# Performance work log

Hardware: AMD Instinct MI355X
Metric: run time of the kernel (lower is better)

## Reference

```python
import jax, jax.numpy as jnp
import numpy as np

N, K = 200000, 16
C_IN = 4           # in_channels (head stage)
H1, H2 = 16, 32    # nbr_hidden_channels//2, nbr_hidden_channels
C_OUT = 64         # channel_list[0]
HEAD = 256         # head_channels
EPS = 1e-5


def _bn(x, g, b):
    # train-mode BatchNorm1d over the row (point/neighbor) axis
    m = jnp.mean(x, axis=0)
    v = jnp.var(x, axis=0)
    return (x - m) * jax.lax.rsqrt(v + EPS) * g + b


def setup_inputs() -> dict:
    key = jax.random.key(0)
    ks = jax.random.split(key, 8)

    def lin(k, fan_in, fan_out):
        bound = 1.0 / np.sqrt(fan_in)  # torch Linear default init
        return jax.random.uniform(k, (fan_in, fan_out), minval=-bound, maxval=bound, dtype=jnp.float32)

    return {
        "p": jax.random.normal(ks[0], (N, 3), dtype=jnp.float32),
        "f": jax.random.normal(ks[1], (N, C_IN), dtype=jnp.float32),
        "group_idx": jax.random.randint(ks[2], (N, K), 0, N),
        "w1": lin(ks[3], 3 + C_IN, H1),
        "g1": jnp.ones((H1,), jnp.float32),
        "b1": jnp.zeros((H1,), jnp.float32),
        "w2": lin(ks[4], H1, H2),
        "g2": jnp.ones((H2,), jnp.float32),
        "b2": jnp.zeros((H2,), jnp.float32),
        "w3": lin(ks[5], H2, C_OUT),
        "g_nbr": 0.8 * jnp.ones((C_OUT,), jnp.float32),  # nn.init.constant_(nbr_bn.weight, 0.8)
        "b_nbr": jnp.zeros((C_OUT,), jnp.float32),
        "g_post": jnp.ones((C_OUT,), jnp.float32),       # (channel_list[0]/out_channels)**0.5 == 1.0
        "b_post": jnp.zeros((C_OUT,), jnp.float32),
        "w_post": lin(ks[6], C_OUT, HEAD),
    }


def reference(p, f, group_idx, w1, g1, b1, w2, g2, b2, w3, g_nbr, b_nbr, g_post, b_post, w_post):
    # neighbor gather: relative coords and features  -> (N, K, 3), (N, K, C_IN)
    p_nbr = p[group_idx] - p[:, None, :]
    f_nbr = f[group_idx]
    x = jnp.concatenate([p_nbr, f_nbr], axis=-1).reshape(N * K, 3 + C_IN)
    # nbr_embed: Linear-BN-GELU x2 + Linear (all no-bias linears)
    x = jax.nn.gelu(_bn(x @ w1, g1, b1), approximate=False)
    x = jax.nn.gelu(_bn(x @ w2, g2, b2), approximate=False)
    x = (x @ w3).reshape(N, K, C_OUT).max(axis=1)  # max-pool over K neighbors
    # nbr_proj is Identity for the head stage; nbr_bn then f = f_nbr
    x = _bn(x, g_nbr, b_nbr)
    # post_proj: BN + Linear(C_OUT -> HEAD, no bias)
    out = _bn(x, g_post, b_post) @ w_post
    return out
```

## Files before the change

kernel.cpp:

```cpp
#include <hip/hip_runtime.h>
#include <cmath>

#define NPTS  200000
#define KNBR  16
#define MROWS 3200000
#define EPSB  1e-5f
#define H2LD  260

__device__ __forceinline__ float gelu_f(float x) {
    return 0.5f * x * (1.0f + erff(x * 0.70710678118654752f));
}

__global__ __launch_bounds__(256) void k_pack(
    const float* __restrict__ p, const float4* __restrict__ f,
    float4* __restrict__ pk)
{
    int n = blockIdx.x * 256 + threadIdx.x;
    if (n < NPTS) {
        float4 a;
        a.x = p[n * 3 + 0]; a.y = p[n * 3 + 1]; a.z = p[n * 3 + 2]; a.w = 0.f;
        pk[2 * n]     = a;
        pk[2 * n + 1] = f[n];
    }
}

__global__ __launch_bounds__(256) void k_stats1(
    const float4* __restrict__ pk, const int* __restrict__ gidx,
    float* __restrict__ stats)
{
    __shared__ float red[4 * 35];

    float acc[35];
#pragma unroll
    for (int c = 0; c < 35; c++) acc[c] = 0.f;

    int stride = gridDim.x * 256;
    for (int r = blockIdx.x * 256 + threadIdx.x; r < MROWS; r += stride) {
        int n = r >> 4;
        int idx = gidx[r];
        float4 pa = pk[2 * idx];
        float4 fb = pk[2 * idx + 1];
        float4 pc = pk[2 * n];
        float x[7];
        x[0] = pa.x - pc.x; x[1] = pa.y - pc.y; x[2] = pa.z - pc.z;
        x[3] = fb.x; x[4] = fb.y; x[5] = fb.z; x[6] = fb.w;
#pragma unroll
        for (int i = 0; i < 7; i++) acc[i] += x[i];
        int t = 7;
#pragma unroll
        for (int i = 0; i < 7; i++)
#pragma unroll
            for (int l = i; l < 7; l++) { acc[t] = fmaf(x[i], x[l], acc[t]); t++; }
    }
    int lane = threadIdx.x & 63, wv = threadIdx.x >> 6;
#pragma unroll
    for (int c = 0; c < 35; c++) {
        float v = acc[c];
        v += __shfl_down(v, 32); v += __shfl_down(v, 16); v += __shfl_down(v, 8);
        v += __shfl_down(v, 4);  v += __shfl_down(v, 2);  v += __shfl_down(v, 1);
        if (lane == 0) red[wv * 35 + c] = v;
    }
    __syncthreads();
    for (int c = threadIdx.x; c < 35; c += 256)
        atomicAdd(&stats[c], red[c] + red[35 + c] + red[70 + c] + red[105 + c]);
}

__global__ void k_fin1(const float* __restrict__ stats, const float* __restrict__ w1,
                       const float* __restrict__ g, const float* __restrict__ b,
                       float* __restrict__ scsh)
{
    int j = threadIdx.x;
    if (j < 16) {
        const float invM = 1.0f / (float)MROWS;
        float w[7];
#pragma unroll
        for (int i = 0; i < 7; i++) w[i] = w1[i * 16 + j];
        float m = 0.f;
#pragma unroll
        for (int i = 0; i < 7; i++) m = fmaf(w[i], stats[i], m);
        m *= invM;
        float e2 = 0.f;
        int t = 7;
#pragma unroll
        for (int i = 0; i < 7; i++)
#pragma unroll
            for (int l = i; l < 7; l++) {
                float coeff = (i == l) ? 1.0f : 2.0f;
                e2 = fmaf(coeff * w[i] * w[l], stats[t], e2);
                t++;
            }
        e2 *= invM;
        float v = e2 - m * m;
        float sc = g[j] * rsqrtf(v + EPSB);
        scsh[j] = sc;
        scsh[16 + j] = fmaf(-m, sc, b[j]);
    }
}

__global__ __launch_bounds__(256) void k_stats2a(
    const float4* __restrict__ pk, const int* __restrict__ gidx,
    const float* __restrict__ w1, const float* __restrict__ scsh1,
    float* __restrict__ stats)
{
    __shared__ __align__(16) float w1s[112];
    __shared__ float sc1s[16], sh1s[16];
    __shared__ float red[4 * 81];
    for (int i = threadIdx.x; i < 112; i += 256) w1s[i] = w1[i];
    if (threadIdx.x < 16) {
        sc1s[threadIdx.x] = scsh1[threadIdx.x];
        sh1s[threadIdx.x] = scsh1[16 + threadIdx.x];
    }
    __syncthreads();
    const float4* w1v = (const float4*)w1s;

    float acc[81];
#pragma unroll
    for (int c = 0; c < 81; c++) acc[c] = 0.f;

    int stride = gridDim.x * 256;
    for (int r = blockIdx.x * 256 + threadIdx.x; r < MROWS; r += stride) {
        int n = r >> 4;
        int idx = gidx[r];
        float4 pa = pk[2 * idx];
        float4 fb = pk[2 * idx + 1];
        float4 pc = pk[2 * n];
        float x[7];
        x[0] = pa.x - pc.x; x[1] = pa.y - pc.y; x[2] = pa.z - pc.z;
        x[3] = fb.x; x[4] = fb.y; x[5] = fb.z; x[6] = fb.w;
        float h1[16];
#pragma unroll
        for (int j0 = 0; j0 < 16; j0 += 4) {
            float y0 = 0.f, y1 = 0.f, y2 = 0.f, y3 = 0.f;
#pragma unroll
            for (int i = 0; i < 7; i++) {
                float4 w = w1v[i * 4 + (j0 >> 2)];
                float xi = x[i];
                y0 = fmaf(xi, w.x, y0); y1 = fmaf(xi, w.y, y1);
                y2 = fmaf(xi, w.z, y2); y3 = fmaf(xi, w.w, y3);
            }
            h1[j0 + 0] = gelu_f(fmaf(y0, sc1s[j0 + 0], sh1s[j0 + 0]));
            h1[j0 + 1] = gelu_f(fmaf(y1, sc1s[j0 + 1], sh1s[j0 + 1]));
            h1[j0 + 2] = gelu_f(fmaf(y2, sc1s[j0 + 2], sh1s[j0 + 2]));
            h1[j0 + 3] = gelu_f(fmaf(y3, sc1s[j0 + 3], sh1s[j0 + 3]));
        }
        int t = 0;
#pragma unroll
        for (int i = 0; i < 6; i++)
#pragma unroll
            for (int l = i; l < 16; l++) { acc[t] = fmaf(h1[i], h1[l], acc[t]); t++; }
    }
    int lane = threadIdx.x & 63, wv = threadIdx.x >> 6;
#pragma unroll
    for (int c = 0; c < 81; c++) {
        float v = acc[c];
        v += __shfl_down(v, 32); v += __shfl_down(v, 16); v += __shfl_down(v, 8);
        v += __shfl_down(v, 4);  v += __shfl_down(v, 2);  v += __shfl_down(v, 1);
        if (lane == 0) red[wv * 81 + c] = v;
    }
    __syncthreads();
    for (int c = threadIdx.x; c < 81; c += 256)
        atomicAdd(&stats[c], red[c] + red[81 + c] + red[162 + c] + red[243 + c]);
}

__global__ __launch_bounds__(256) void k_stats2b(
    const float4* __restrict__ pk, const int* __restrict__ gidx,
    const float* __restrict__ w1, const float* __restrict__ scsh1,
    float* __restrict__ stats)
{
    __shared__ __align__(16) float w1s[112];
    __shared__ float sc1s[16], sh1s[16];
    __shared__ float red[4 * 71];
    for (int i = threadIdx.x; i < 112; i += 256) w1s[i] = w1[i];
    if (threadIdx.x < 16) {
        sc1s[threadIdx.x] = scsh1[threadIdx.x];
        sh1s[threadIdx.x] = scsh1[16 + threadIdx.x];
    }
    __syncthreads();
    const float4* w1v = (const float4*)w1s;

    float acc[71];
#pragma unroll
    for (int c = 0; c < 71; c++) acc[c] = 0.f;

    int stride = gridDim.x * 256;
    for (int r = blockIdx.x * 256 + threadIdx.x; r < MROWS; r += stride) {
        int n = r >> 4;
        int idx = gidx[r];
        float4 pa = pk[2 * idx];
        float4 fb = pk[2 * idx + 1];
        float4 pc = pk[2 * n];
        float x[7];
        x[0] = pa.x - pc.x; x[1] = pa.y - pc.y; x[2] = pa.z - pc.z;
        x[3] = fb.x; x[4] = fb.y; x[5] = fb.z; x[6] = fb.w;
        float h1[16];
#pragma unroll
        for (int j0 = 0; j0 < 16; j0 += 4) {
            float y0 = 0.f, y1 = 0.f, y2 = 0.f, y3 = 0.f;
#pragma unroll
            for (int i = 0; i < 7; i++) {
                float4 w = w1v[i * 4 + (j0 >> 2)];
                float xi = x[i];
                y0 = fmaf(xi, w.x, y0); y1 = fmaf(xi, w.y, y1);
                y2 = fmaf(xi, w.z, y2); y3 = fmaf(xi, w.w, y3);
            }
            h1[j0 + 0] = gelu_f(fmaf(y0, sc1s[j0 + 0], sh1s[j0 + 0]));
            h1[j0 + 1] = gelu_f(fmaf(y1, sc1s[j0 + 1], sh1s[j0 + 1]));
            h1[j0 + 2] = gelu_f(fmaf(y2, sc1s[j0 + 2], sh1s[j0 + 2]));
            h1[j0 + 3] = gelu_f(fmaf(y3, sc1s[j0 + 3], sh1s[j0 + 3]));
        }
#pragma unroll
        for (int i = 0; i < 16; i++) acc[i] += h1[i];
        int t = 16;
#pragma unroll
        for (int i = 6; i < 16; i++)
#pragma unroll
            for (int l = i; l < 16; l++) { acc[t] = fmaf(h1[i], h1[l], acc[t]); t++; }
    }
    int lane = threadIdx.x & 63, wv = threadIdx.x >> 6;
#pragma unroll
    for (int c = 0; c < 71; c++) {
        float v = acc[c];
        v += __shfl_down(v, 32); v += __shfl_down(v, 16); v += __shfl_down(v, 8);
        v += __shfl_down(v, 4);  v += __shfl_down(v, 2);  v += __shfl_down(v, 1);
        if (lane == 0) red[wv * 71 + c] = v;
    }
    __syncthreads();
    for (int c = threadIdx.x; c < 71; c += 256)
        atomicAdd(&stats[81 + c], red[c] + red[71 + c] + red[142 + c] + red[213 + c]);
}

__global__ void k_fin2(const float* __restrict__ stats, const float* __restrict__ w2,
                       const float* __restrict__ g, const float* __restrict__ b,
                       float* __restrict__ scsh)
{
    int j = threadIdx.x;
    if (j < 32) {
        const float invM = 1.0f / (float)MROWS;
        float w[16];
#pragma unroll
        for (int i = 0; i < 16; i++) w[i] = w2[i * 32 + j];
        float m = 0.f;
#pragma unroll
        for (int i = 0; i < 16; i++) m = fmaf(w[i], stats[81 + i], m);
        m *= invM;
        float e2 = 0.f;
        int t = 0;
#pragma unroll
        for (int i = 0; i < 6; i++)
#pragma unroll
            for (int l = i; l < 16; l++) {
                float coeff = (i == l) ? 1.0f : 2.0f;
                e2 = fmaf(coeff * w[i] * w[l], stats[t], e2);
                t++;
            }
        t = 97;
#pragma unroll
        for (int i = 6; i < 16; i++)
#pragma unroll
            for (int l = i; l < 16; l++) {
                float coeff = (i == l) ? 1.0f : 2.0f;
                e2 = fmaf(coeff * w[i] * w[l], stats[t], e2);
                t++;
            }
        e2 *= invM;
        float v = e2 - m * m;
        float sc = g[j] * rsqrtf(v + EPSB);
        scsh[j] = sc;
        scsh[32 + j] = fmaf(-m, sc, b[j]);
    }
}

__global__ __launch_bounds__(256) void k_pool2(
    const float* __restrict__ p, const float4* __restrict__ f,
    const int* __restrict__ gidx,
    const float* __restrict__ w1, const float* __restrict__ w2,
    const float* __restrict__ w3,
    const float* __restrict__ scsh1, const float* __restrict__ scsh2,
    float* __restrict__ stats, float* __restrict__ pooled)
{
    __shared__ __align__(16) float w1s[112];
    __shared__ __align__(16) float w2s[512];
    __shared__ __align__(16) float w3s[2048];
    __shared__ __align__(16) float h2t[32 * H2LD];
    __shared__ float sc1s[16], sh1s[16], sc2s[32], sh2s[32];
    __shared__ float reds[256];
    __shared__ float redq[256];
    int tid = threadIdx.x;
    for (int i = tid; i < 112; i += 256) w1s[i] = w1[i];
    for (int i = tid; i < 512; i += 256) w2s[i] = w2[i];
    for (int i = tid; i < 2048; i += 256) w3s[i] = w3[i];
    if (tid < 16) { sc1s[tid] = scsh1[tid]; sh1s[tid] = scsh1[16 + tid]; }
    if (tid < 32) { sc2s[tid] = scsh2[tid]; sh2s[tid] = scsh2[32 + tid]; }
    __syncthreads();

    const float4* w1v = (const float4*)w1s;
    const float4* w2v = (const float4*)w2s;
    const float4* w3v = (const float4*)w3s;

    int lane = tid & 63;
    int pt = tid >> 4;
    int cc = tid & 15;

    float s0 = 0.f, s1 = 0.f, s2 = 0.f, s3 = 0.f;
    float q0 = 0.f, q1 = 0.f, q2 = 0.f, q3 = 0.f;

#pragma unroll 1
    for (int it = 0; it < 4; it++) {
        int r = it * 800000 + blockIdx.x * 256 + tid;
        int n = r >> 4;
        int idx = gidx[r];
        float4 fv = f[idx];
        float x[7];
        x[0] = p[idx * 3 + 0] - p[n * 3 + 0];
        x[1] = p[idx * 3 + 1] - p[n * 3 + 1];
        x[2] = p[idx * 3 + 2] - p[n * 3 + 2];
        x[3] = fv.x; x[4] = fv.y; x[5] = fv.z; x[6] = fv.w;

        float h1[16];
#pragma unroll
        for (int j0 = 0; j0 < 16; j0 += 4) {
            float y0 = 0.f, y1 = 0.f, y2 = 0.f, y3 = 0.f;
#pragma unroll
            for (int i = 0; i < 7; i++) {
                float4 w = w1v[i * 4 + (j0 >> 2)];
                float xi = x[i];
                y0 = fmaf(xi, w.x, y0); y1 = fmaf(xi, w.y, y1);
                y2 = fmaf(xi, w.z, y2); y3 = fmaf(xi, w.w, y3);
            }
            h1[j0 + 0] = gelu_f(fmaf(y0, sc1s[j0 + 0], sh1s[j0 + 0]));
            h1[j0 + 1] = gelu_f(fmaf(y1, sc1s[j0 + 1], sh1s[j0 + 1]));
            h1[j0 + 2] = gelu_f(fmaf(y2, sc1s[j0 + 2], sh1s[j0 + 2]));
            h1[j0 + 3] = gelu_f(fmaf(y3, sc1s[j0 + 3], sh1s[j0 + 3]));
        }
#pragma unroll
        for (int j0 = 0; j0 < 32; j0 += 4) {
            float y0 = 0.f, y1 = 0.f, y2 = 0.f, y3 = 0.f;
#pragma unroll
            for (int i = 0; i < 16; i++) {
                float4 w = w2v[i * 8 + (j0 >> 2)];
                float hi = h1[i];
                y0 = fmaf(hi, w.x, y0); y1 = fmaf(hi, w.y, y1);
                y2 = fmaf(hi, w.z, y2); y3 = fmaf(hi, w.w, y3);
            }
            h2t[(j0 + 0) * H2LD + tid] = gelu_f(fmaf(y0, sc2s[j0 + 0], sh2s[j0 + 0]));
            h2t[(j0 + 1) * H2LD + tid] = gelu_f(fmaf(y1, sc2s[j0 + 1], sh2s[j0 + 1]));
            h2t[(j0 + 2) * H2LD + tid] = gelu_f(fmaf(y2, sc2s[j0 + 2], sh2s[j0 + 2]));
            h2t[(j0 + 3) * H2LD + tid] = gelu_f(fmaf(y3, sc2s[j0 + 3], sh2s[j0 + 3]));
        }
        __syncthreads();

        float m0 = -3.0e38f, m1 = -3.0e38f, m2 = -3.0e38f, m3 = -3.0e38f;
#pragma unroll 1
        for (int qd = 0; qd < 4; qd++) {
            int rb = (pt << 4) + (qd << 2);
            float a00 = 0.f, a01 = 0.f, a02 = 0.f, a03 = 0.f;
            float a10 = 0.f, a11 = 0.f, a12 = 0.f, a13 = 0.f;
            float a20 = 0.f, a21 = 0.f, a22 = 0.f, a23 = 0.f;
            float a30 = 0.f, a31 = 0.f, a32 = 0.f, a33 = 0.f;
#pragma unroll 8
            for (int i = 0; i < 32; i++) {
                float4 hv = *(const float4*)&h2t[i * H2LD + rb];
                float4 wf = w3v[i * 16 + cc];
                a00 = fmaf(hv.x, wf.x, a00); a01 = fmaf(hv.x, wf.y, a01);
                a02 = fmaf(hv.x, wf.z, a02); a03 = fmaf(hv.x, wf.w, a03);
                a10 = fmaf(hv.y, wf.x, a10); a11 = fmaf(hv.y, wf.y, a11);
                a12 = fmaf(hv.y, wf.z, a12); a13 = fmaf(hv.y, wf.w, a13);
                a20 = fmaf(hv.z, wf.x, a20); a21 = fmaf(hv.z, wf.y, a21);
                a22 = fmaf(hv.z, wf.z, a22); a23 = fmaf(hv.z, wf.w, a23);
                a30 = fmaf(hv.w, wf.x, a30); a31 = fmaf(hv.w, wf.y, a31);
                a32 = fmaf(hv.w, wf.z, a32); a33 = fmaf(hv.w, wf.w, a33);
            }
            m0 = fmaxf(fmaxf(fmaxf(m0, a00), fmaxf(a10, a20)), a30);
            m1 = fmaxf(fmaxf(fmaxf(m1, a01), fmaxf(a11, a21)), a31);
            m2 = fmaxf(fmaxf(fmaxf(m2, a02), fmaxf(a12, a22)), a32);
            m3 = fmaxf(fmaxf(fmaxf(m3, a03), fmaxf(a13, a23)), a33);
        }
        int np = it * 50000 + blockIdx.x * 16 + pt;
        *(float4*)&pooled[(size_t)np * 64 + cc * 4] = make_float4(m0, m1, m2, m3);
        s0 += m0; q0 = fmaf(m0, m0, q0);
        s1 += m1; q1 = fmaf(m1, m1, q1);
        s2 += m2; q2 = fmaf(m2, m2, q2);
        s3 += m3; q3 = fmaf(m3, m3, q3);
        __syncthreads();
    }

    s0 += __shfl_down(s0, 32); s0 += __shfl_down(s0, 16);
    s1 += __shfl_down(s1, 32); s1 += __shfl_down(s1, 16);
    s2 += __shfl_down(s2, 32); s2 += __shfl_down(s2, 16);
    s3 += __shfl_down(s3, 32); s3 += __shfl_down(s3, 16);
    q0 += __shfl_down(q0, 32); q0 += __shfl_down(q0, 16);
    q1 += __shfl_down(q1, 32); q1 += __shfl_down(q1, 16);
    q2 += __shfl_down(q2, 32); q2 += __shfl_down(q2, 16);
    q3 += __shfl_down(q3, 32); q3 += __shfl_down(q3, 16);
    int wv = tid >> 6;
    if (lane < 16) {
        reds[wv * 64 + lane * 4 + 0] = s0;
        reds[wv * 64 + lane * 4 + 1] = s1;
        reds[wv * 64 + lane * 4 + 2] = s2;
        reds[wv * 64 + lane * 4 + 3] = s3;
        redq[wv * 64 + lane * 4 + 0] = q0;
        redq[wv * 64 + lane * 4 + 1] = q1;
        redq[wv * 64 + lane * 4 + 2] = q2;
        redq[wv * 64 + lane * 4 + 3] = q3;
    }
    __syncthreads();
    if (tid < 64) {
        atomicAdd(&stats[tid],
                  reds[tid] + reds[64 + tid] + reds[128 + tid] + reds[192 + tid]);
        atomicAdd(&stats[64 + tid],
                  redq[tid] + redq[64 + tid] + redq[128 + tid] + redq[192 + tid]);
    }
}

__global__ void k_fin3(const float* __restrict__ stats,
                       const float* __restrict__ g_nbr, const float* __restrict__ g_post,
                       const float* __restrict__ b_post, float* __restrict__ scsh)
{
    int j = threadIdx.x;
    if (j < 64) {
        float m = stats[j] * (1.0f / NPTS);
        float v = stats[64 + j] * (1.0f / NPTS) - m * m;
        float a1 = g_nbr[j] * rsqrtf(v + EPSB);
        float s3 = g_post[j] * a1 * rsqrtf(fmaf(a1 * a1, v, EPSB));
        scsh[j] = s3;
        scsh[64 + j] = fmaf(-m, s3, b_post[j]);
    }
}

__global__ __launch_bounds__(256) void k_head(
    const float* __restrict__ pooled, const float* __restrict__ scsh3,
    const float* __restrict__ wpost, float* __restrict__ out)
{
    __shared__ float rowbuf[512];
    __shared__ float s3s[64], c3s[64];
    int tid = threadIdx.x;
    if (tid < 64) { s3s[tid] = scsh3[tid]; c3s[tid] = scsh3[64 + tid]; }
    float wcol[64];
#pragma unroll
    for (int j = 0; j < 64; j++) wcol[j] = wpost[j * 256 + tid];
    __syncthreads();

    const int nchunks = NPTS / 8;
    for (int c = blockIdx.x; c < nchunks; c += gridDim.x) {
        int n0 = c * 8;
#pragma unroll
        for (int t = tid; t < 512; t += 256) {
            int rr = t >> 6, j = t & 63;
            rowbuf[t] = fmaf(pooled[(size_t)(n0 + rr) * 64 + j], s3s[j], c3s[j]);
        }
        __syncthreads();
#pragma unroll
        for (int rr = 0; rr < 8; rr++) {
            float acc = 0.f;
#pragma unroll
            for (int j = 0; j < 64; j++) acc = fmaf(rowbuf[rr * 64 + j], wcol[j], acc);
            out[(size_t)(n0 + rr) * 256 + tid] = acc;
        }
        __syncthreads();
    }
}

extern "C" void kernel_launch(void* const* d_in, const int* in_sizes, int n_in,
                              void* d_out, int out_size, void* d_ws, size_t ws_size,
                              hipStream_t stream)
{
    const float*  p    = (const float*)d_in[0];
    const float4* f    = (const float4*)d_in[1];
    const int*    gidx = (const int*)d_in[2];
    const float*  w1   = (const float*)d_in[3];
    const float*  g1   = (const float*)d_in[4];
    const float*  b1   = (const float*)d_in[5];
    const float*  w2   = (const float*)d_in[6];
    const float*  g2   = (const float*)d_in[7];
    const float*  b2   = (const float*)d_in[8];
    const float*  w3   = (const float*)d_in[9];
    const float*  gn   = (const float*)d_in[10];
    const float*  gp   = (const float*)d_in[12];
    const float*  bp   = (const float*)d_in[13];
    const float*  wp   = (const float*)d_in[14];
    float* out = (float*)d_out;
    float* ws  = (float*)d_ws;

    float* stats1 = ws;
    float* scsh1  = ws + 40;
    float* stats2 = ws + 80;
    float* scsh2  = ws + 240;
    float* stats3 = ws + 304;
    float* scsh3  = ws + 432;
    float* pooled = ws + 1024;
    float4* pk    = (float4*)(ws + 1024);

    hipMemsetAsync(d_ws, 0, 2048, stream);
    k_pack<<<(NPTS + 255) / 256, 256, 0, stream>>>(p, f, pk);
    k_stats1<<<2048, 256, 0, stream>>>(pk, gidx, stats1);
    k_fin1<<<1, 64, 0, stream>>>(stats1, w1, g1, b1, scsh1);
    k_stats2a<<<2048, 256, 0, stream>>>(pk, gidx, w1, scsh1, stats2);
    k_stats2b<<<2048, 256, 0, stream>>>(pk, gidx, w1, scsh1, stats2);
    k_fin2<<<1, 64, 0, stream>>>(stats2, w2, g2, b2, scsh2);
    k_pool2<<<3125, 256, 0, stream>>>(p, f, gidx, w1, w2, w3, scsh1, scsh2, stats3, pooled);
    k_fin3<<<1, 64, 0, stream>>>(stats3, gn, gp, bp, scsh3);
    k_head<<<1024, 256, 0, stream>>>(pooled, scsh3, wp, out);
}
```

Measured before the change: 1.287 ms.

## Materialize first-layer pre-activations once and reuse across stats and pool passes

The first linear layer's 16-channel output per neighbor row is computed once and stored in workspace in a transposed, coalesced layout. The layer-1 BN statistics now come directly from per-channel sums instead of the 7x7 input moment trick. The later moment passes and the pooling kernel read this buffer instead of repeating the random neighbor gather and layer-1 matmul. In exchange the code writes and then reads about 205 MB of extra traffic three times, and falls back to the old gather path when the workspace is too small.

```diff
diff --git a/kernel.cpp b/kernel.cpp
--- a/kernel.cpp
+++ b/kernel.cpp
@@ -24,18 +24,25 @@
     }
 }
 
-__global__ __launch_bounds__(256) void k_stats1(
+__global__ __launch_bounds__(256) void k_gy1(
     const float4* __restrict__ pk, const int* __restrict__ gidx,
-    float* __restrict__ stats)
-{
-    __shared__ float red[4 * 35];
-
-    float acc[35];
-#pragma unroll
-    for (int c = 0; c < 35; c++) acc[c] = 0.f;
-
+    const float* __restrict__ w1, float* __restrict__ stats,
+    float* __restrict__ y1d)
+{
+    __shared__ __align__(16) float w1s[112];
+    __shared__ float red[4 * 32];
+    for (int i = threadIdx.x; i < 112; i += 256) w1s[i] = w1[i];
+    __syncthreads();
+    const float4* w1v = (const float4*)w1s;
+
+    float acc[32];
+#pragma unroll
+    for (int c = 0; c < 32; c++) acc[c] = 0.f;
+
+    int tid = threadIdx.x;
+    int lr = tid & 63;
     int stride = gridDim.x * 256;
-    for (int r = blockIdx.x * 256 + threadIdx.x; r < MROWS; r += stride) {
+    for (int r = blockIdx.x * 256 + tid; r < MROWS; r += stride) {
         int n = r >> 4;
         int idx = gidx[r];
         float4 pa = pk[2 * idx];
@@ -44,90 +51,7 @@
         float x[7];
         x[0] = pa.x - pc.x; x[1] = pa.y - pc.y; x[2] = pa.z - pc.z;
         x[3] = fb.x; x[4] = fb.y; x[5] = fb.z; x[6] = fb.w;
-#pragma unroll
-        for (int i = 0; i < 7; i++) acc[i] += x[i];
-        int t = 7;
-#pragma unroll
-        for (int i = 0; i < 7; i++)
-#pragma unroll
-            for (int l = i; l < 7; l++) { acc[t] = fmaf(x[i], x[l], acc[t]); t++; }
-    }
-    int lane = threadIdx.x & 63, wv = threadIdx.x >> 6;
-#pragma unroll
-    for (int c = 0; c < 35; c++) {
-        float v = acc[c];
-        v += __shfl_down(v, 32); v += __shfl_down(v, 16); v += __shfl_down(v, 8);
-        v += __shfl_down(v, 4);  v += __shfl_down(v, 2);  v += __shfl_down(v, 1);
-        if (lane == 0) red[wv * 35 + c] = v;
-    }
-    __syncthreads();
-    for (int c = threadIdx.x; c < 35; c += 256)
-        atomicAdd(&stats[c], red[c] + red[35 + c] + red[70 + c] + red[105 + c]);
-}
-
-__global__ void k_fin1(const float* __restrict__ stats, const float* __restrict__ w1,
-                       const float* __restrict__ g, const float* __restrict__ b,
-                       float* __restrict__ scsh)
-{
-    int j = threadIdx.x;
-    if (j < 16) {
-        const float invM = 1.0f / (float)MROWS;
-        float w[7];
-#pragma unroll
-        for (int i = 0; i < 7; i++) w[i] = w1[i * 16 + j];
-        float m = 0.f;
-#pragma unroll
-        for (int i = 0; i < 7; i++) m = fmaf(w[i], stats[i], m);
-        m *= invM;
-        float e2 = 0.f;
-        int t = 7;
-#pragma unroll
-        for (int i = 0; i < 7; i++)
-#pragma unroll
-            for (int l = i; l < 7; l++) {
-                float coeff = (i == l) ? 1.0f : 2.0f;
-                e2 = fmaf(coeff * w[i] * w[l], stats[t], e2);
-                t++;
-            }
-        e2 *= invM;
-        float v = e2 - m * m;
-        float sc = g[j] * rsqrtf(v + EPSB);
-        scsh[j] = sc;
-        scsh[16 + j] = fmaf(-m, sc, b[j]);
-    }
-}
-
-__global__ __launch_bounds__(256) void k_stats2a(
-    const float4* __restrict__ pk, const int* __restrict__ gidx,
-    const float* __restrict__ w1, const float* __restrict__ scsh1,
-    float* __restrict__ stats)
-{
-    __shared__ __align__(16) float w1s[112];
-    __shared__ float sc1s[16], sh1s[16];
-    __shared__ float red[4 * 81];
-    for (int i = threadIdx.x; i < 112; i += 256) w1s[i] = w1[i];
-    if (threadIdx.x < 16) {
-        sc1s[threadIdx.x] = scsh1[threadIdx.x];
-        sh1s[threadIdx.x] = scsh1[16 + threadIdx.x];
-    }
-    __syncthreads();
-    const float4* w1v = (const float4*)w1s;
-
-    float acc[81];
-#pragma unroll
-    for (int c = 0; c < 81; c++) acc[c] = 0.f;
-
-    int stride = gridDim.x * 256;
-    for (int r = blockIdx.x * 256 + threadIdx.x; r < MROWS; r += stride) {
-        int n = r >> 4;
-        int idx = gidx[r];
-        float4 pa = pk[2 * idx];
-        float4 fb = pk[2 * idx + 1];
-        float4 pc = pk[2 * n];
-        float x[7];
-        x[0] = pa.x - pc.x; x[1] = pa.y - pc.y; x[2] = pa.z - pc.z;
-        x[3] = fb.x; x[4] = fb.y; x[5] = fb.z; x[6] = fb.w;
-        float h1[16];
+        float* yb = y1d + (size_t)(r >> 6) * 1024 + lr;
 #pragma unroll
         for (int j0 = 0; j0 < 16; j0 += 4) {
             float y0 = 0.f, y1 = 0.f, y2 = 0.f, y3 = 0.f;
@@ -138,18 +62,73 @@
                 y0 = fmaf(xi, w.x, y0); y1 = fmaf(xi, w.y, y1);
                 y2 = fmaf(xi, w.z, y2); y3 = fmaf(xi, w.w, y3);
             }
-            h1[j0 + 0] = gelu_f(fmaf(y0, sc1s[j0 + 0], sh1s[j0 + 0]));
-            h1[j0 + 1] = gelu_f(fmaf(y1, sc1s[j0 + 1], sh1s[j0 + 1]));
-            h1[j0 + 2] = gelu_f(fmaf(y2, sc1s[j0 + 2], sh1s[j0 + 2]));
-            h1[j0 + 3] = gelu_f(fmaf(y3, sc1s[j0 + 3], sh1s[j0 + 3]));
-        }
+            yb[(j0 + 0) * 64] = y0; yb[(j0 + 1) * 64] = y1;
+            yb[(j0 + 2) * 64] = y2; yb[(j0 + 3) * 64] = y3;
+            acc[j0 + 0] += y0; acc[16 + j0 + 0] += y0 * y0;
+            acc[j0 + 1] += y1; acc[16 + j0 + 1] += y1 * y1;
+            acc[j0 + 2] += y2; acc[16 + j0 + 2] += y2 * y2;
+            acc[j0 + 3] += y3; acc[16 + j0 + 3] += y3 * y3;
+        }
+    }
+    int lane = tid & 63, wv = tid >> 6;
+#pragma unroll
+    for (int c = 0; c < 32; c++) {
+        float v = acc[c];
+        v += __shfl_down(v, 32); v += __shfl_down(v, 16); v += __shfl_down(v, 8);
+        v += __shfl_down(v, 4);  v += __shfl_down(v, 2);  v += __shfl_down(v, 1);
+        if (lane == 0) red[wv * 32 + c] = v;
+    }
+    __syncthreads();
+    for (int c = tid; c < 32; c += 256)
+        atomicAdd(&stats[c], red[c] + red[32 + c] + red[64 + c] + red[96 + c]);
+}
+
+__global__ void k_fin1b(const float* __restrict__ stats, const float* __restrict__ g,
+                        const float* __restrict__ b, float* __restrict__ scsh)
+{
+    int j = threadIdx.x;
+    if (j < 16) {
+        const float invM = 1.0f / (float)MROWS;
+        float m = stats[j] * invM;
+        float v = stats[16 + j] * invM - m * m;
+        float sc = g[j] * rsqrtf(v + EPSB);
+        scsh[j] = sc;
+        scsh[16 + j] = fmaf(-m, sc, b[j]);
+    }
+}
+
+__global__ __launch_bounds__(256) void k_momA(
+    const float* __restrict__ y1d, const float* __restrict__ scsh1,
+    float* __restrict__ stats)
+{
+    __shared__ float sc1s[16], sh1s[16];
+    __shared__ float red[4 * 81];
+    if (threadIdx.x < 16) {
+        sc1s[threadIdx.x] = scsh1[threadIdx.x];
+        sh1s[threadIdx.x] = scsh1[16 + threadIdx.x];
+    }
+    __syncthreads();
+
+    float acc[81];
+#pragma unroll
+    for (int c = 0; c < 81; c++) acc[c] = 0.f;
+
+    int tid = threadIdx.x;
+    int lr = tid & 63;
+    int stride = gridDim.x * 256;
+    for (int r = blockIdx.x * 256 + tid; r < MROWS; r += stride) {
+        const float* yb = y1d + (size_t)(r >> 6) * 1024 + lr;
+        float h1[16];
+#pragma unroll
+        for (int j = 0; j < 16; j++)
+            h1[j] = gelu_f(fmaf(yb[j * 64], sc1s[j], sh1s[j]));
         int t = 0;
 #pragma unroll
         for (int i = 0; i < 6; i++)
 #pragma unroll
             for (int l = i; l < 16; l++) { acc[t] = fmaf(h1[i], h1[l], acc[t]); t++; }
     }
-    int lane = threadIdx.x & 63, wv = threadIdx.x >> 6;
+    int lane = tid & 63, wv = tid >> 6;
 #pragma unroll
     for (int c = 0; c < 81; c++) {
         float v = acc[c];
@@ -158,56 +137,35 @@
         if (lane == 0) red[wv * 81 + c] = v;
     }
     __syncthreads();
-    for (int c = threadIdx.x; c < 81; c += 256)
+    for (int c = tid; c < 81; c += 256)
         atomicAdd(&stats[c], red[c] + red[81 + c] + red[162 + c] + red[243 + c]);
 }
 
-__global__ __launch_bounds__(256) void k_stats2b(
-    const float4* __restrict__ pk, const int* __restrict__ gidx,
-    const float* __restrict__ w1, const float* __restrict__ scsh1,
+__global__ __launch_bounds__(256) void k_momB(
+    const float* __restrict__ y1d, const float* __restrict__ scsh1,
     float* __restrict__ stats)
 {
-    __shared__ __align__(16) float w1s[112];
     __shared__ float sc1s[16], sh1s[16];
     __shared__ float red[4 * 71];
-    for (int i = threadIdx.x; i < 112; i += 256) w1s[i] = w1[i];
     if (threadIdx.x < 16) {
         sc1s[threadIdx.x] = scsh1[threadIdx.x];
         sh1s[threadIdx.x] = scsh1[16 + threadIdx.x];
     }
     __syncthreads();
-    const float4* w1v = (const float4*)w1s;
 
     float acc[71];
 #pragma unroll
     for (int c = 0; c < 71; c++) acc[c] = 0.f;
 
+    int tid = threadIdx.x;
+    int lr = tid & 63;
     int stride = gridDim.x * 256;
-    for (int r = blockIdx.x * 256 + threadIdx.x; r < MROWS; r += stride) {
-        int n = r >> 4;
-        int idx = gidx[r];
-        float4 pa = pk[2 * idx];
-        float4 fb = pk[2 * idx + 1];
-        float4 pc = pk[2 * n];
-        float x[7];
-        x[0] = pa.x - pc.x; x[1] = pa.y - pc.y; x[2] = pa.z - pc.z;
-        x[3] = fb.x; x[4] = fb.y; x[5] = fb.z; x[6] = fb.w;
+    for (int r = blockIdx.x * 256 + tid; r < MROWS; r += stride) {
+        const float* yb = y1d + (size_t)(r >> 6) * 1024 + lr;
         float h1[16];
 #pragma unroll
-        for (int j0 = 0; j0 < 16; j0 += 4) {
-            float y0 = 0.f, y1 = 0.f, y2 = 0.f, y3 = 0.f;
-#pragma unroll
-            for (int i = 0; i < 7; i++) {
-                float4 w = w1v[i * 4 + (j0 >> 2)];
-                float xi = x[i];
-                y0 = fmaf(xi, w.x, y0); y1 = fmaf(xi, w.y, y1);
-                y2 = fmaf(xi, w.z, y2); y3 = fmaf(xi, w.w, y3);
-            }
-            h1[j0 + 0] = gelu_f(fmaf(y0, sc1s[j0 + 0], sh1s[j0 + 0]));
-            h1[j0 + 1] = gelu_f(fmaf(y1, sc1s[j0 + 1], sh1s[j0 + 1]));
-            h1[j0 + 2] = gelu_f(fmaf(y2, sc1s[j0 + 2], sh1s[j0 + 2]));
-            h1[j0 + 3] = gelu_f(fmaf(y3, sc1s[j0 + 3], sh1s[j0 + 3]));
-        }
+        for (int j = 0; j < 16; j++)
+            h1[j] = gelu_f(fmaf(yb[j * 64], sc1s[j], sh1s[j]));
 #pragma unroll
         for (int i = 0; i < 16; i++) acc[i] += h1[i];
         int t = 16;
@@ -216,7 +174,7 @@
 #pragma unroll
             for (int l = i; l < 16; l++) { acc[t] = fmaf(h1[i], h1[l], acc[t]); t++; }
     }
-    int lane = threadIdx.x & 63, wv = threadIdx.x >> 6;
+    int lane = tid & 63, wv = tid >> 6;
 #pragma unroll
     for (int c = 0; c < 71; c++) {
         float v = acc[c];
@@ -225,7 +183,7 @@
         if (lane == 0) red[wv * 71 + c] = v;
     }
     __syncthreads();
-    for (int c = threadIdx.x; c < 71; c += 256)
+    for (int c = tid; c < 71; c += 256)
         atomicAdd(&stats[81 + c], red[c] + red[71 + c] + red[142 + c] + red[213 + c]);
 }
 
@@ -270,15 +228,12 @@
     }
 }
 
-__global__ __launch_bounds__(256) void k_pool2(
-    const float* __restrict__ p, const float4* __restrict__ f,
-    const int* __restrict__ gidx,
-    const float* __restrict__ w1, const float* __restrict__ w2,
-    const float* __restrict__ w3,
+__global__ __launch_bounds__(256) void k_pool2y(
+    const float* __restrict__ y1d,
+    const float* __restrict__ w2, const float* __restrict__ w3,
     const float* __restrict__ scsh1, const float* __restrict__ scsh2,
     float* __restrict__ stats, float* __restrict__ pooled)
 {
-    __shared__ __align__(16) float w1s[112];
     __shared__ __align__(16) float w2s[512];
     __shared__ __align__(16) float w3s[2048];
     __shared__ __align__(16) float h2t[32 * H2LD];
@@ -286,14 +241,12 @@
     __shared__ float reds[256];
     __shared__ float redq[256];
     int tid = threadIdx.x;
-    for (int i = tid; i < 112; i += 256) w1s[i] = w1[i];
     for (int i = tid; i < 512; i += 256) w2s[i] = w2[i];
     for (int i = tid; i < 2048; i += 256) w3s[i] = w3[i];
     if (tid < 16) { sc1s[tid] = scsh1[tid]; sh1s[tid] = scsh1[16 + tid]; }
     if (tid < 32) { sc2s[tid] = scsh2[tid]; sh2s[tid] = scsh2[32 + tid]; }
     __syncthreads();
 
-    const float4* w1v = (const float4*)w1s;
     const float4* w2v = (const float4*)w2s;
     const float4* w3v = (const float4*)w3s;
 
@@ -307,31 +260,11 @@
 #pragma unroll 1
     for (int it = 0; it < 4; it++) {
         int r = it * 800000 + blockIdx.x * 256 + tid;
-        int n = r >> 4;
-        int idx = gidx[r];
-        float4 fv = f[idx];
-        float x[7];
-        x[0] = p[idx * 3 + 0] - p[n * 3 + 0];
-        x[1] = p[idx * 3 + 1] - p[n * 3 + 1];
-        x[2] = p[idx * 3 + 2] - p[n * 3 + 2];
-        x[3] = fv.x; x[4] = fv.y; x[5] = fv.z; x[6] = fv.w;
-
+        const float* yb = y1d + (size_t)(r >> 6) * 1024 + lane;
         float h1[16];
 #pragma unroll
-        for (int j0 = 0; j0 < 16; j0 += 4) {
-            float y0 = 0.f, y1 = 0.f, y2 = 0.f, y3 = 0.f;
-#pragma unroll
-            for (int i = 0; i < 7; i++) {
-                float4 w = w1v[i * 4 + (j0 >> 2)];
-                float xi = x[i];
-                y0 = fmaf(xi, w.x, y0); y1 = fmaf(xi, w.y, y1);
-                y2 = fmaf(xi, w.z, y2); y3 = fmaf(xi, w.w, y3);
-            }
-            h1[j0 + 0] = gelu_f(fmaf(y0, sc1s[j0 + 0], sh1s[j0 + 0]));
-            h1[j0 + 1] = gelu_f(fmaf(y1, sc1s[j0 + 1], sh1s[j0 + 1]));
-            h1[j0 + 2] = gelu_f(fmaf(y2, sc1s[j0 + 2], sh1s[j0 + 2]));
-            h1[j0 + 3] = gelu_f(fmaf(y3, sc1s[j0 + 3], sh1s[j0 + 3]));
-        }
+        for (int j = 0; j < 16; j++)
+            h1[j] = gelu_f(fmaf(yb[j * 64], sc1s[j], sh1s[j]));
 #pragma unroll
         for (int j0 = 0; j0 < 32; j0 += 4) {
             float y0 = 0.f, y1 = 0.f, y2 = 0.f, y3 = 0.f;
@@ -412,6 +345,297 @@
     }
 }
 
+__global__ __launch_bounds__(256) void k_s1g(
+    const float4* __restrict__ pk, const int* __restrict__ gidx,
+    float* __restrict__ stats)
+{
+    __shared__ float red[4 * 35];
+    float acc[35];
+#pragma unroll
+    for (int c = 0; c < 35; c++) acc[c] = 0.f;
+    int stride = gridDim.x * 256;
+    for (int r = blockIdx.x * 256 + threadIdx.x; r < MROWS; r += stride) {
+        int n = r >> 4;
+        int idx = gidx[r];
+        float4 pa = pk[2 * idx];
+        float4 fb = pk[2 * idx + 1];
+        float4 pc = pk[2 * n];
+        float x[7];
+        x[0] = pa.x - pc.x; x[1] = pa.y - pc.y; x[2] = pa.z - pc.z;
+        x[3] = fb.x; x[4] = fb.y; x[5] = fb.z; x[6] = fb.w;
+#pragma unroll
+        for (int i = 0; i < 7; i++) acc[i] += x[i];
+        int t = 7;
+#pragma unroll
+        for (int i = 0; i < 7; i++)
+#pragma unroll
+            for (int l = i; l < 7; l++) { acc[t] = fmaf(x[i], x[l], acc[t]); t++; }
+    }
+    int lane = threadIdx.x & 63, wv = threadIdx.x >> 6;
+#pragma unroll
+    for (int c = 0; c < 35; c++) {
+        float v = acc[c];
+        v += __shfl_down(v, 32); v += __shfl_down(v, 16); v += __shfl_down(v, 8);
+        v += __shfl_down(v, 4);  v += __shfl_down(v, 2);  v += __shfl_down(v, 1);
+        if (lane == 0) red[wv * 35 + c] = v;
+    }
+    __syncthreads();
+    for (int c = threadIdx.x; c < 35; c += 256)
+        atomicAdd(&stats[c], red[c] + red[35 + c] + red[70 + c] + red[105 + c]);
+}
+
+__global__ void k_f1g(const float* __restrict__ stats, const float* __restrict__ w1,
+                      const float* __restrict__ g, const float* __restrict__ b,
+                      float* __restrict__ scsh)
+{
+    int j = threadIdx.x;
+    if (j < 16) {
+        const float invM = 1.0f / (float)MROWS;
+        float w[7];
+#pragma unroll
+        for (int i = 0; i < 7; i++) w[i] = w1[i * 16 + j];
+        float m = 0.f;
+#pragma unroll
+        for (int i = 0; i < 7; i++) m = fmaf(w[i], stats[i], m);
+        m *= invM;
+        float e2 = 0.f;
+        int t = 7;
+#pragma unroll
+        for (int i = 0; i < 7; i++)
+#pragma unroll
+            for (int l = i; l < 7; l++) {
+                float coeff = (i == l) ? 1.0f : 2.0f;
+                e2 = fmaf(coeff * w[i] * w[l], stats[t], e2);
+                t++;
+            }
+        e2 *= invM;
+        float v = e2 - m * m;
+        float sc = g[j] * rsqrtf(v + EPSB);
+        scsh[j] = sc;
+        scsh[16 + j] = fmaf(-m, sc, b[j]);
+    }
+}
+
+template <int PASS>
+__global__ __launch_bounds__(256) void k_s2g(
+    const float4* __restrict__ pk, const int* __restrict__ gidx,
+    const float* __restrict__ w1, const float* __restrict__ scsh1,
+    float* __restrict__ stats)
+{
+    constexpr int NA = (PASS == 0) ? 81 : 71;
+    __shared__ __align__(16) float w1s[112];
+    __shared__ float sc1s[16], sh1s[16];
+    __shared__ float red[4 * NA];
+    for (int i = threadIdx.x; i < 112; i += 256) w1s[i] = w1[i];
+    if (threadIdx.x < 16) {
+        sc1s[threadIdx.x] = scsh1[threadIdx.x];
+        sh1s[threadIdx.x] = scsh1[16 + threadIdx.x];
+    }
+    __syncthreads();
+    const float4* w1v = (const float4*)w1s;
+
+    float acc[NA];
+#pragma unroll
+    for (int c = 0; c < NA; c++) acc[c] = 0.f;
+
+    int stride = gridDim.x * 256;
+    for (int r = blockIdx.x * 256 + threadIdx.x; r < MROWS; r += stride) {
+        int n = r >> 4;
+        int idx = gidx[r];
+        float4 pa = pk[2 * idx];
+        float4 fb = pk[2 * idx + 1];
+        float4 pc = pk[2 * n];
+        float x[7];
+        x[0] = pa.x - pc.x; x[1] = pa.y - pc.y; x[2] = pa.z - pc.z;
+        x[3] = fb.x; x[4] = fb.y; x[5] = fb.z; x[6] = fb.w;
+        float h1[16];
+#pragma unroll
+        for (int j0 = 0; j0 < 16; j0 += 4) {
+            float y0 = 0.f, y1 = 0.f, y2 = 0.f, y3 = 0.f;
+#pragma unroll
+            for (int i = 0; i < 7; i++) {
+                float4 w = w1v[i * 4 + (j0 >> 2)];
+                float xi = x[i];
+                y0 = fmaf(xi, w.x, y0); y1 = fmaf(xi, w.y, y1);
+                y2 = fmaf(xi, w.z, y2); y3 = fmaf(xi, w.w, y3);
+            }
+            h1[j0 + 0] = gelu_f(fmaf(y0, sc1s[j0 + 0], sh1s[j0 + 0]));
+            h1[j0 + 1] = gelu_f(fmaf(y1, sc1s[j0 + 1], sh1s[j0 + 1]));
+            h1[j0 + 2] = gelu_f(fmaf(y2, sc1s[j0 + 2], sh1s[j0 + 2]));
+            h1[j0 + 3] = gelu_f(fmaf(y3, sc1s[j0 + 3], sh1s[j0 + 3]));
+        }
+        if (PASS == 0) {
+            int t = 0;
+#pragma unroll
+            for (int i = 0; i < 6; i++)
+#pragma unroll
+                for (int l = i; l < 16; l++) { acc[t] = fmaf(h1[i], h1[l], acc[t]); t++; }
+        } else {
+#pragma unroll
+            for (int i = 0; i < 16; i++) acc[i] += h1[i];
+            int t = 16;
+#pragma unroll
+            for (int i = 6; i < 16; i++)
+#pragma unroll
+                for (int l = i; l < 16; l++) { acc[t] = fmaf(h1[i], h1[l], acc[t]); t++; }
+        }
+    }
+    int lane = threadIdx.x & 63, wv = threadIdx.x >> 6;
+#pragma unroll
+    for (int c = 0; c < NA; c++) {
+        float v = acc[c];
+        v += __shfl_down(v, 32); v += __shfl_down(v, 16); v += __shfl_down(v, 8);
+        v += __shfl_down(v, 4);  v += __shfl_down(v, 2);  v += __shfl_down(v, 1);
+        if (lane == 0) red[wv * NA + c] = v;
+    }
+    __syncthreads();
+    int base = (PASS == 0) ? 0 : 81;
+    for (int c = threadIdx.x; c < NA; c += 256)
+        atomicAdd(&stats[base + c], red[c] + red[NA + c] + red[2 * NA + c] + red[3 * NA + c]);
+}
+
+__global__ __launch_bounds__(256) void k_pool2g(
+    const float* __restrict__ p, const float4* __restrict__ f,
+    const int* __restrict__ gidx,
+    const float* __restrict__ w1, const float* __restrict__ w2,
+    const float* __restrict__ w3,
+    const float* __restrict__ scsh1, const float* __restrict__ scsh2,
+    float* __restrict__ stats, float* __restrict__ pooled)
+{
+    __shared__ __align__(16) float w1s[112];
+    __shared__ __align__(16) float w2s[512];
+    __shared__ __align__(16) float w3s[2048];
+    __shared__ __align__(16) float h2t[32 * H2LD];
+    __shared__ float sc1s[16], sh1s[16], sc2s[32], sh2s[32];
+    __shared__ float reds[256];
+    __shared__ float redq[256];
+    int tid = threadIdx.x;
+    for (int i = tid; i < 112; i += 256) w1s[i] = w1[i];
+    for (int i = tid; i < 512; i += 256) w2s[i] = w2[i];
+    for (int i = tid; i < 2048; i += 256) w3s[i] = w3[i];
+    if (tid < 16) { sc1s[tid] = scsh1[tid]; sh1s[tid] = scsh1[16 + tid]; }
+    if (tid < 32) { sc2s[tid] = scsh2[tid]; sh2s[tid] = scsh2[32 + tid]; }
+    __syncthreads();
+
+    const float4* w1v = (const float4*)w1s;
+    const float4* w2v = (const float4*)w2s;
+    const float4* w3v = (const float4*)w3s;
+
+    int lane = tid & 63;
+    int pt = tid >> 4;
+    int cc = tid & 15;
+
+    float s0 = 0.f, s1 = 0.f, s2 = 0.f, s3 = 0.f;
+    float q0 = 0.f, q1 = 0.f, q2 = 0.f, q3 = 0.f;
+
+#pragma unroll 1
+    for (int it = 0; it < 4; it++) {
+        int r = it * 800000 + blockIdx.x * 256 + tid;
+        int n = r >> 4;
+        int idx = gidx[r];
+        float4 fv = f[idx];
+        float x[7];
+        x[0] = p[idx * 3 + 0] - p[n * 3 + 0];
+        x[1] = p[idx * 3 + 1] - p[n * 3 + 1];
+        x[2] = p[idx * 3 + 2] - p[n * 3 + 2];
+        x[3] = fv.x; x[4] = fv.y; x[5] = fv.z; x[6] = fv.w;
+
+        float h1[16];
+#pragma unroll
+        for (int j0 = 0; j0 < 16; j0 += 4) {
+            float y0 = 0.f, y1 = 0.f, y2 = 0.f, y3 = 0.f;
+#pragma unroll
+            for (int i = 0; i < 7; i++) {
+                float4 w = w1v[i * 4 + (j0 >> 2)];
+                float xi = x[i];
+                y0 = fmaf(xi, w.x, y0); y1 = fmaf(xi, w.y, y1);
+                y2 = fmaf(xi, w.z, y2); y3 = fmaf(xi, w.w, y3);
+            }
+            h1[j0 + 0] = gelu_f(fmaf(y0, sc1s[j0 + 0], sh1s[j0 + 0]));
+            h1[j0 + 1] = gelu_f(fmaf(y1, sc1s[j0 + 1], sh1s[j0 + 1]));
+            h1[j0 + 2] = gelu_f(fmaf(y2, sc1s[j0 + 2], sh1s[j0 + 2]));
+            h1[j0 + 3] = gelu_f(fmaf(y3, sc1s[j0 + 3], sh1s[j0 + 3]));
+        }
+#pragma unroll
+        for (int j0 = 0; j0 < 32; j0 += 4) {
+            float y0 = 0.f, y1 = 0.f, y2 = 0.f, y3 = 0.f;
+#pragma unroll
+            for (int i = 0; i < 16; i++) {
+                float4 w = w2v[i * 8 + (j0 >> 2)];
+                float hi = h1[i];
+                y0 = fmaf(hi, w.x, y0); y1 = fmaf(hi, w.y, y1);
+                y2 = fmaf(hi, w.z, y2); y3 = fmaf(hi, w.w, y3);
+            }
+            h2t[(j0 + 0) * H2LD + tid] = gelu_f(fmaf(y0, sc2s[j0 + 0], sh2s[j0 + 0]));
+            h2t[(j0 + 1) * H2LD + tid] = gelu_f(fmaf(y1, sc2s[j0 + 1], sh2s[j0 + 1]));
+            h2t[(j0 + 2) * H2LD + tid] = gelu_f(fmaf(y2, sc2s[j0 + 2], sh2s[j0 + 2]));
+            h2t[(j0 + 3) * H2LD + tid] = gelu_f(fmaf(y3, sc2s[j0 + 3], sh2s[j0 + 3]));
+        }
+        __syncthreads();
+
+        float m0 = -3.0e38f, m1 = -3.0e38f, m2 = -3.0e38f, m3 = -3.0e38f;
+#pragma unroll 1
+        for (int qd = 0; qd < 4; qd++) {
+            int rb = (pt << 4) + (qd << 2);
+            float a00 = 0.f, a01 = 0.f, a02 = 0.f, a03 = 0.f;
+            float a10 = 0.f, a11 = 0.f, a12 = 0.f, a13 = 0.f;
+            float a20 = 0.f, a21 = 0.f, a22 = 0.f, a23 = 0.f;
+            float a30 = 0.f, a31 = 0.f, a32 = 0.f, a33 = 0.f;
+#pragma unroll 8
+            for (int i = 0; i < 32; i++) {
+                float4 hv = *(const float4*)&h2t[i * H2LD + rb];
+                float4 wf = w3v[i * 16 + cc];
+                a00 = fmaf(hv.x, wf.x, a00); a01 = fmaf(hv.x, wf.y, a01);
+                a02 = fmaf(hv.x, wf.z, a02); a03 = fmaf(hv.x, wf.w, a03);
+                a10 = fmaf(hv.y, wf.x, a10); a11 = fmaf(hv.y, wf.y, a11);
+                a12 = fmaf(hv.y, wf.z, a12); a13 = fmaf(hv.y, wf.w, a13);
+                a20 = fmaf(hv.z, wf.x, a20); a21 = fmaf(hv.z, wf.y, a21);
+                a22 = fmaf(hv.z, wf.z, a22); a23 = fmaf(hv.z, wf.w, a23);
+                a30 = fmaf(hv.w, wf.x, a30); a31 = fmaf(hv.w, wf.y, a31);
+                a32 = fmaf(hv.w, wf.z, a32); a33 = fmaf(hv.w, wf.w, a33);
+            }
+            m0 = fmaxf(fmaxf(fmaxf(m0, a00), fmaxf(a10, a20)), a30);
+            m1 = fmaxf(fmaxf(fmaxf(m1, a01), fmaxf(a11, a21)), a31);
+            m2 = fmaxf(fmaxf(fmaxf(m2, a02), fmaxf(a12, a22)), a32);
+            m3 = fmaxf(fmaxf(fmaxf(m3, a03), fmaxf(a13, a23)), a33);
+        }
+        int np = it * 50000 + blockIdx.x * 16 + pt;
+        *(float4*)&pooled[(size_t)np * 64 + cc * 4] = make_float4(m0, m1, m2, m3);
+        s0 += m0; q0 = fmaf(m0, m0, q0);
+        s1 += m1; q1 = fmaf(m1, m1, q1);
+        s2 += m2; q2 = fmaf(m2, m2, q2);
+        s3 += m3; q3 = fmaf(m3, m3, q3);
+        __syncthreads();
+    }
+
+    s0 += __shfl_down(s0, 32); s0 += __shfl_down(s0, 16);
+    s1 += __shfl_down(s1, 32); s1 += __shfl_down(s1, 16);
+    s2 += __shfl_down(s2, 32); s2 += __shfl_down(s2, 16);
+    s3 += __shfl_down(s3, 32); s3 += __shfl_down(s3, 16);
+    q0 += __shfl_down(q0, 32); q0 += __shfl_down(q0, 16);
+    q1 += __shfl_down(q1, 32); q1 += __shfl_down(q1, 16);
+    q2 += __shfl_down(q2, 32); q2 += __shfl_down(q2, 16);
+    q3 += __shfl_down(q3, 32); q3 += __shfl_down(q3, 16);
+    int wv = tid >> 6;
+    if (lane < 16) {
+        reds[wv * 64 + lane * 4 + 0] = s0;
+        reds[wv * 64 + lane * 4 + 1] = s1;
+        reds[wv * 64 + lane * 4 + 2] = s2;
+        reds[wv * 64 + lane * 4 + 3] = s3;
+        redq[wv * 64 + lane * 4 + 0] = q0;
+        redq[wv * 64 + lane * 4 + 1] = q1;
+        redq[wv * 64 + lane * 4 + 2] = q2;
+        redq[wv * 64 + lane * 4 + 3] = q3;
+    }
+    __syncthreads();
+    if (tid < 64) {
+        atomicAdd(&stats[tid],
+                  reds[tid] + reds[64 + tid] + reds[128 + tid] + reds[192 + tid]);
+        atomicAdd(&stats[64 + tid],
+                  redq[tid] + redq[64 + tid] + redq[128 + tid] + redq[192 + tid]);
+    }
+}
+
 __global__ void k_fin3(const float* __restrict__ stats,
                        const float* __restrict__ g_nbr, const float* __restrict__ g_post,
                        const float* __restrict__ b_post, float* __restrict__ scsh)
@@ -489,15 +713,28 @@
     float* scsh3  = ws + 432;
     float* pooled = ws + 1024;
     float4* pk    = (float4*)(ws + 1024);
+    float* y1d    = ws + 1024 + 12800000;
+
+    const size_t need = ((size_t)1024 + 12800000 + 51200000) * 4;
 
     hipMemsetAsync(d_ws, 0, 2048, stream);
     k_pack<<<(NPTS + 255) / 256, 256, 0, stream>>>(p, f, pk);
-    k_stats1<<<2048, 256, 0, stream>>>(pk, gidx, stats1);
-    k_fin1<<<1, 64, 0, stream>>>(stats1, w1, g1, b1, scsh1);
-    k_stats2a<<<2048, 256, 0, stream>>>(pk, gidx, w1, scsh1, stats2);
-    k_stats2b<<<2048, 256, 0, stream>>>(pk, gidx, w1, scsh1, stats2);
-    k_fin2<<<1, 64, 0, stream>>>(stats2, w2, g2, b2, scsh2);
-    k_pool2<<<3125, 256, 0, stream>>>(p, f, gidx, w1, w2, w3, scsh1, scsh2, stats3, pooled);
+
+    if (ws_size >= need) {
+        k_gy1<<<2048, 256, 0, stream>>>(pk, gidx, w1, stats1, y1d);
+        k_fin1b<<<1, 64, 0, stream>>>(stats1, g1, b1, scsh1);
+        k_momA<<<2048, 256, 0, stream>>>(y1d, scsh1, stats2);
+        k_momB<<<2048, 256, 0, stream>>>(y1d, scsh1, stats2);
+        k_fin2<<<1, 64, 0, stream>>>(stats2, w2, g2, b2, scsh2);
+        k_pool2y<<<3125, 256, 0, stream>>>(y1d, w2, w3, scsh1, scsh2, stats3, pooled);
+    } else {
+        k_s1g<<<2048, 256, 0, stream>>>(pk, gidx, stats1);
+        k_f1g<<<1, 64, 0, stream>>>(stats1, w1, g1, b1, scsh1);
+        k_s2g<0><<<2048, 256, 0, stream>>>(pk, gidx, w1, scsh1, stats2);
+        k_s2g<1><<<2048, 256, 0, stream>>>(pk, gidx, w1, scsh1, stats2);
+        k_fin2<<<1, 64, 0, stream>>>(stats2, w2, g2, b2, scsh2);
+        k_pool2g<<<3125, 256, 0, stream>>>(p, f, gidx, w1, w2, w3, scsh1, scsh2, stats3, pooled);
+    }
     k_fin3<<<1, 64, 0, stream>>>(stats3, gn, gp, bp, scsh3);
     k_head<<<1024, 256, 0, stream>>>(pooled, scsh3, wp, out);
 }
```

New measurement: 1.281 ms. Within noise of the previous version (-0.4%).
